# Kernel tuning notes

Hardware: AMD Instinct MI355X
Metric: run time of the kernel (lower is better)

The kernel has to match this reference:

```python
import jax, jax.numpy as jnp
import numpy as np

N, E, G = 50000, 1600000, 512
IN, H = 16, 128


def setup_inputs() -> dict:
    key = jax.random.key(0)
    ks = jax.random.split(key, 10)
    x = jax.random.normal(ks[0], (N, IN), dtype=jnp.float32)
    edge_index = jax.random.randint(ks[1], (2, E), 0, N, dtype=jnp.int64)
    batch = jnp.sort(jax.random.randint(ks[2], (N,), 0, G, dtype=jnp.int64))
    s = lambda k, sh, fan: jax.random.normal(k, sh, dtype=jnp.float32) / np.sqrt(fan)
    return {
        "x": x, "edge_index": edge_index, "batch": batch,
        "W1": s(ks[3], (IN, H), IN), "b1": jnp.zeros((H,), jnp.float32),
        "W2": s(ks[4], (H, H), H), "b2": jnp.zeros((H,), jnp.float32),
        "Wlab": s(ks[5], (H, 1), H), "blab": jnp.zeros((1,), jnp.float32),
        "Wd1": s(ks[6], (H, 64), H), "bd1": jnp.zeros((64,), jnp.float32),
        "Wd2": s(ks[7], (64, 2), 64), "bd2": jnp.zeros((2,), jnp.float32),
    }


def _gcn_conv(x, src, dst, norm, W, b, num_nodes):
    # x' = sum_{(s,d) in E+selfloops} norm_e * (x W)[s] scattered to d, + b
    h = x @ W                                  # [N, H]
    msgs = h[src] * norm[:, None]              # [E+N, H]
    out = jax.ops.segment_sum(msgs, dst, num_segments=num_nodes)
    return out + b


def _forward(x, edge_index, batch, W1, b1, W2, b2, Wlab, blab, Wd1, bd1, Wd2, bd2):
    num_nodes = x.shape[0]
    loop = jnp.arange(num_nodes, dtype=edge_index.dtype)
    src = jnp.concatenate([edge_index[0], loop])
    dst = jnp.concatenate([edge_index[1], loop])
    # symmetric GCN normalization: deg computed at dst after self-loops
    deg = jax.ops.segment_sum(jnp.ones_like(dst, dtype=x.dtype), dst,
                              num_segments=num_nodes)
    dinv = jnp.where(deg > 0, jax.lax.rsqrt(deg), 0.0)
    norm = dinv[src] * dinv[dst]               # [E+N]

    h = jax.nn.relu(_gcn_conv(x, src, dst, norm, W1, b1, num_nodes))
    h = jax.nn.relu(_gcn_conv(h, src, dst, norm, W2, b2, num_nodes))

    # global mean pool over graphs
    sums = jax.ops.segment_sum(h, batch, num_segments=G)        # [G, H]
    cnts = jax.ops.segment_sum(jnp.ones((num_nodes,), h.dtype), batch,
                               num_segments=G)
    pooled = sums / jnp.maximum(cnts, 1.0)[:, None]

    label_out = jax.nn.sigmoid(pooled @ Wlab + blab)            # [G, 1]
    # grad_reverse is identity in the forward pass
    dom_out = jax.nn.relu(pooled @ Wd1 + bd1) @ Wd2 + bd2       # [G, 2]
    return label_out, dom_out


def reference(x, edge_index, batch, W1, b1, W2, b2, Wlab, blab, Wd1, bd1, Wd2, bd2):
    return _forward(x, edge_index, batch, W1, b1, W2, b2, Wlab, blab,
                    Wd1, bd1, Wd2, bd2)
```

## Files before the change

### kernel.cpp

```cpp
#include <hip/hip_runtime.h>
#include <math.h>


#define BCAP 12288

typedef __attribute__((ext_vector_type(8))) short short8;
typedef __attribute__((ext_vector_type(4))) float f32x4;

__device__ __forceinline__ void bf4acc(uint2 u, float* a) {
    a[0] += __uint_as_float(u.x << 16);
    a[1] += __uint_as_float(u.x & 0xffff0000u);
    a[2] += __uint_as_float(u.y << 16);
    a[3] += __uint_as_float(u.y & 0xffff0000u);
}

__device__ __forceinline__ void bf8acc(uint4 u, float* a) {
    a[0] += __uint_as_float(u.x << 16);
    a[1] += __uint_as_float(u.x & 0xffff0000u);
    a[2] += __uint_as_float(u.y << 16);
    a[3] += __uint_as_float(u.y & 0xffff0000u);
    a[4] += __uint_as_float(u.z << 16);
    a[5] += __uint_as_float(u.z & 0xffff0000u);
    a[6] += __uint_as_float(u.w << 16);
    a[7] += __uint_as_float(u.w & 0xffff0000u);
}

__device__ __forceinline__ unsigned short bf1(float a) {
    unsigned ua = __float_as_uint(a);
    return (unsigned short)((ua + 0x7fffu + ((ua >> 16) & 1u)) >> 16);
}

__global__ __launch_bounds__(256) void k_bfill(
        const int* __restrict__ ei, int* __restrict__ bcnt,
        unsigned* __restrict__ col1,
        const int* __restrict__ batch, int* __restrict__ gptr,
        float* __restrict__ gsum, const float* __restrict__ W2,
        unsigned short* __restrict__ W2bf,
        int E, int chunk, int NB, int N, int G) {
    __shared__ int bins[256];
    __shared__ int base[256];
    for (int t = threadIdx.x; t < NB; t += 256) bins[t] = 0;
    __syncthreads();
    const int e0 = blockIdx.x * chunk;
    int e1 = e0 + chunk; if (e1 > E) e1 = E;
    for (int j = e0 + (int)threadIdx.x; j < e1; j += 256)
        atomicAdd(&bins[ei[E + j] >> 8], 1);
    __syncthreads();
    for (int t = threadIdx.x; t < NB; t += 256) {
        base[t] = bins[t] ? atomicAdd(&bcnt[t], bins[t]) : 0;
        bins[t] = 0;
    }
    __syncthreads();
    for (int j = e0 + (int)threadIdx.x; j < e1; j += 256) {
        int d = ei[E + j];
        int s = ei[j];
        int b = d >> 8;
        int pos = base[b] + atomicAdd(&bins[b], 1);
        if (pos < BCAP)
            col1[(size_t)b * BCAP + pos] = ((unsigned)(d & 255) << 16) | (unsigned)s;
    }

    const int gid = blockIdx.x * 256 + threadIdx.x;
    const int gsz = gridDim.x * 256;
    for (int i = gid; i < G * 32; i += gsz)
        ((float4*)gsum)[i] = make_float4(0.f, 0.f, 0.f, 0.f);
    for (int i = gid; i < 16384; i += gsz) {
        const int f2 = i >> 7, f1 = i & 127;
        W2bf[i] = bf1(W2[f1 * 128 + f2]);
    }
    for (int g = gid; g <= G; g += gsz) {
        int lo = 0, hi = N;
        while (lo < hi) {
            int mid = (lo + hi) >> 1;
            if (batch[mid] < g) lo = mid + 1; else hi = mid;
        }
        gptr[g] = lo;
    }
}

__global__ __launch_bounds__(256) void k_bsort(const unsigned* __restrict__ col1,
                                               const int* __restrict__ bcnt,
                                               int* __restrict__ col,
                                               int* __restrict__ rowptr,
                                               float* __restrict__ dinv,
                                               const float* __restrict__ x,
                                               unsigned short* __restrict__ xsb,
                                               int N, int E, int NB) {
    __shared__ unsigned ec[BCAP];
    __shared__ int bins[256], sc[256];
    __shared__ float dvb[256];
    const int b = blockIdx.x, t = threadIdx.x;

    {
        int v = (t < NB) ? bcnt[t] : 0;
        bins[t] = v;
        __syncthreads();
        for (int off = 1; off < 256; off <<= 1) {
            int add = (t >= off) ? bins[t - off] : 0;
            __syncthreads();
            bins[t] += add;
            __syncthreads();
        }
    }
    const int s0 = (b == 0) ? 0 : bins[b - 1];
    int cnt = bcnt[b];
    if (cnt > BCAP) cnt = BCAP;
    __syncthreads();

    for (int i = t; i < cnt; i += 256) ec[i] = col1[(size_t)b * BCAP + i];
    bins[t] = 0;
    __syncthreads();
    for (int i = t; i < cnt; i += 256) atomicAdd(&bins[ec[i] >> 16], 1);
    __syncthreads();
    const int v = bins[t];
    sc[t] = v;
    __syncthreads();
    for (int off = 1; off < 256; off <<= 1) {
        int add = (t >= off) ? sc[t - off] : 0;
        __syncthreads();
        sc[t] += add;
        __syncthreads();
    }
    const int ex = sc[t] - v;
    __syncthreads();
    sc[t] = ex;
    bins[t] = 0;
    const float dv = rsqrtf((float)(v + 1));
    dvb[t] = dv;
    const int n0 = b * 256;
    if (n0 + t < N) {
        rowptr[n0 + t] = s0 + ex;
        dinv[n0 + t] = dv;
    }
    if (b == 0 && t == 0) rowptr[N] = E;
    __syncthreads();
    for (int i = t; i < cnt; i += 256) {
        unsigned e = ec[i];
        int dl = e >> 16;
        int p = sc[dl] + atomicAdd(&bins[dl], 1);
        col[s0 + p] = (int)(e & 0xffffu);
    }
    int nn = N - n0; if (nn > 256) nn = 256;
    const int lim = nn * 16;
    for (int i = t; i < lim; i += 256) {
        float vx = x[(size_t)n0 * 16 + i] * dvb[i >> 4];
        xsb[(size_t)n0 * 16 + i] = bf1(vx);
    }
}

__global__ __launch_bounds__(512, 4) void k_l12g(
        const int* __restrict__ rowptr, const int* __restrict__ col,
        const unsigned short* __restrict__ xsb,
        const float* __restrict__ dinv,
        const float* __restrict__ W1, const float* __restrict__ b1,
        const unsigned short* __restrict__ W2bf,
        unsigned short* __restrict__ ht1b, int N) {
    __shared__ __align__(16) unsigned short W2s[128 * 136];
    __shared__ __align__(16) unsigned short h1b[64 * 136];
    __shared__ __align__(16) float arow[64 * 16];
    __shared__ float dv[64];
    const int tid = threadIdx.x;
    const int n0 = blockIdx.x * 64;
    const int w = tid >> 6, lane = tid & 63;

    for (int i = tid; i < 2048; i += 512) {
        const int f2 = i >> 4, seg = i & 15;
        *(uint4*)&W2s[f2 * 136 + seg * 8] = ((const uint4*)W2bf)[i];
    }
    if (tid < 64) dv[tid] = (n0 + tid < N) ? dinv[n0 + tid] : 0.f;

    {
        const int nd = lane >> 3, sub = lane & 7;
        const int slot = sub >> 2, qq = sub & 3;
        const int j = w * 8 + nd;
        const int n = n0 + j;
        float a[4] = {0.f, 0.f, 0.f, 0.f};
        if (n < N) {
            const int r1 = rowptr[n + 1];
            for (int e = rowptr[n] + slot; e < r1; e += 2)
                bf4acc(*(const uint2*)(xsb + (size_t)col[e] * 16 + qq * 4), a);
        }
#pragma unroll
        for (int i = 0; i < 4; ++i) a[i] += __shfl_xor(a[i], 4);
        if (slot == 0) {
            if (n < N) {
                bf4acc(*(const uint2*)(xsb + (size_t)n * 16 + qq * 4), a);
                *(float4*)&arow[j * 16 + qq * 4] = make_float4(a[0], a[1], a[2], a[3]);
            } else {
                *(float4*)&arow[j * 16 + qq * 4] = make_float4(0.f, 0.f, 0.f, 0.f);
            }
        }
    }
    const int f = tid & 127, jg = tid >> 7;
    float w1r[16];
#pragma unroll
    for (int k = 0; k < 16; ++k) w1r[k] = W1[k * 128 + f];
    const float bias = b1[f];
    __syncthreads();

#pragma unroll 4
    for (int j = jg * 16; j < jg * 16 + 16; ++j) {
        float s = 0.f;
#pragma unroll
        for (int k = 0; k < 16; ++k) s += arow[j * 16 + k] * w1r[k];
        h1b[j * 136 + f] = bf1(fmaxf(dv[j] * s + bias, 0.f));
    }
    __syncthreads();

    const int mt = w & 3, nh = w >> 2;
    const int lm = lane & 15, quad = lane >> 4;
    f32x4 acc[4];
#pragma unroll
    for (int t = 0; t < 4; ++t) acc[t] = (f32x4){0.f, 0.f, 0.f, 0.f};
#pragma unroll
    for (int kb = 0; kb < 4; ++kb) {
        const short8 af = *(const short8*)&h1b[(mt * 16 + lm) * 136 + kb * 32 + quad * 8];
#pragma unroll
        for (int t = 0; t < 4; ++t) {
            const short8 bfv = *(const short8*)&W2s[(nh * 64 + t * 16 + lm) * 136 + kb * 32 + quad * 8];
            acc[t] = __builtin_amdgcn_mfma_f32_16x16x32_bf16(af, bfv, acc[t], 0, 0, 0);
        }
    }
#pragma unroll
    for (int t = 0; t < 4; ++t) {
        const int f2 = nh * 64 + t * 16 + lm;
#pragma unroll
        for (int r = 0; r < 4; ++r) {
            const int j = mt * 16 + quad * 4 + r;
            const int n = n0 + j;
            if (n < N)
                ht1b[(size_t)n * 128 + f2] = bf1(acc[t][r] * dv[j]);
        }
    }
}

__global__ __launch_bounds__(512) void k_gat64pool(
        const int* __restrict__ rowptr, const int* __restrict__ col,
        const unsigned short* __restrict__ ht1b,
        const float* __restrict__ dinv, const float* __restrict__ b2,
        const int* __restrict__ batch, float* __restrict__ gsum,
        int N, int c0) {
    __shared__ __align__(16) float h2s[8][64];
    __shared__ int bats[8];
    const int wave = threadIdx.x >> 6, lane = threadIdx.x & 63;
    const int oct = lane >> 3, t8 = lane & 7;
    const int n = blockIdx.x * 8 + wave;
    const unsigned short* hb = ht1b + c0 + t8 * 8;
    float a[8] = {0.f, 0.f, 0.f, 0.f, 0.f, 0.f, 0.f, 0.f};
    if (n < N) {
        const int r1 = rowptr[n + 1];
        int j = rowptr[n] + oct;
        while (j + 24 < r1) {
            const int s0 = col[j], s1 = col[j + 8];
            const int s2 = col[j + 16], s3 = col[j + 24];
            const uint4 u0 = *(const uint4*)(hb + (size_t)s0 * 128);
            const uint4 u1 = *(const uint4*)(hb + (size_t)s1 * 128);
            const uint4 u2 = *(const uint4*)(hb + (size_t)s2 * 128);
            const uint4 u3 = *(const uint4*)(hb + (size_t)s3 * 128);
            bf8acc(u0, a); bf8acc(u1, a); bf8acc(u2, a); bf8acc(u3, a);
            j += 32;
        }
        while (j < r1) {
            bf8acc(*(const uint4*)(hb + (size_t)col[j] * 128), a);
            j += 8;
        }
        if (oct == 0)
            bf8acc(*(const uint4*)(hb + (size_t)n * 128), a);
    }
#pragma unroll
    for (int i = 0; i < 8; ++i) {
        a[i] += __shfl_xor(a[i], 8);
        a[i] += __shfl_xor(a[i], 16);
        a[i] += __shfl_xor(a[i], 32);
    }
    if (oct == 0) {
        if (n < N) {
            const float d = dinv[n];
            const float4 bb0 = *(const float4*)(b2 + c0 + t8 * 8);
            const float4 bb1 = *(const float4*)(b2 + c0 + t8 * 8 + 4);
            const float4 v0 = make_float4(fmaxf(a[0] * d + bb0.x, 0.f),
                                          fmaxf(a[1] * d + bb0.y, 0.f),
                                          fmaxf(a[2] * d + bb0.z, 0.f),
                                          fmaxf(a[3] * d + bb0.w, 0.f));
            const float4 v1 = make_float4(fmaxf(a[4] * d + bb1.x, 0.f),
                                          fmaxf(a[5] * d + bb1.y, 0.f),
                                          fmaxf(a[6] * d + bb1.z, 0.f),
                                          fmaxf(a[7] * d + bb1.w, 0.f));
            *(float4*)&h2s[wave][t8 * 8] = v0;
            *(float4*)&h2s[wave][t8 * 8 + 4] = v1;
            if (t8 == 0) bats[wave] = batch[n];
        } else {
            *(float4*)&h2s[wave][t8 * 8] = make_float4(0.f, 0.f, 0.f, 0.f);
            *(float4*)&h2s[wave][t8 * 8 + 4] = make_float4(0.f, 0.f, 0.f, 0.f);
            if (t8 == 0) bats[wave] = -1;
        }
    }
    __syncthreads();
    if (threadIdx.x < 16) {
        const int qq = threadIdx.x;
        int bprev = bats[0];
        float4 acc4 = *(const float4*)&h2s[0][qq * 4];
#pragma unroll
        for (int wv = 1; wv < 8; ++wv) {
            const int bw = bats[wv];
            const float4 rv = *(const float4*)&h2s[wv][qq * 4];
            if (bw == bprev) {
                acc4.x += rv.x; acc4.y += rv.y; acc4.z += rv.z; acc4.w += rv.w;
            } else {
                if (bprev >= 0) {
                    float* gs = gsum + (size_t)bprev * 128 + c0 + qq * 4;
                    unsafeAtomicAdd(gs + 0, acc4.x); unsafeAtomicAdd(gs + 1, acc4.y);
                    unsafeAtomicAdd(gs + 2, acc4.z); unsafeAtomicAdd(gs + 3, acc4.w);
                }
                bprev = bw; acc4 = rv;
            }
        }
        if (bprev >= 0) {
            float* gs = gsum + (size_t)bprev * 128 + c0 + qq * 4;
            unsafeAtomicAdd(gs + 0, acc4.x); unsafeAtomicAdd(gs + 1, acc4.y);
            unsafeAtomicAdd(gs + 2, acc4.z); unsafeAtomicAdd(gs + 3, acc4.w);
        }
    }
}

__global__ __launch_bounds__(128) void k_head(
        const float* __restrict__ gsum, const int* __restrict__ gptr,
        const float* __restrict__ Wlab, const float* __restrict__ blab,
        const float* __restrict__ Wd1, const float* __restrict__ bd1,
        const float* __restrict__ Wd2, const float* __restrict__ bd2,
        float* __restrict__ out, int G) {
    __shared__ float sp[128];
    __shared__ float red[128];
    __shared__ float hd[64];
    const int g = blockIdx.x, t = threadIdx.x;
    const float cnt = (float)(gptr[g + 1] - gptr[g]);
    const float invc = 1.f / fmaxf(cnt, 1.f);
    const float pooled = gsum[g * 128 + t] * invc;
    sp[t] = pooled;
    red[t] = pooled * Wlab[t];
    __syncthreads();
    for (int off = 64; off > 0; off >>= 1) {
        if (t < off) red[t] += red[t + off];
        __syncthreads();
    }
    if (t == 0) {
        float z = red[0] + blab[0];
        out[g] = 1.f / (1.f + expf(-z));
    }
    if (t < 64) {
        float s = bd1[t];
        for (int f = 0; f < 128; ++f) s += sp[f] * Wd1[f * 64 + t];
        hd[t] = fmaxf(s, 0.f);
    }
    __syncthreads();
    if (t < 2) {
        float s = bd2[t];
        for (int j = 0; j < 64; ++j) s += hd[j] * Wd2[j * 2 + t];
        out[G + g * 2 + t] = s;
    }
}

extern "C" void kernel_launch(void* const* d_in, const int* in_sizes, int n_in,
                              void* d_out, int out_size, void* d_ws, size_t ws_size,
                              hipStream_t stream) {
    const float* x     = (const float*)d_in[0];
    const int*   ei    = (const int*)d_in[1];
    const int*   batch = (const int*)d_in[2];
    const float* W1    = (const float*)d_in[3];
    const float* b1    = (const float*)d_in[4];
    const float* W2    = (const float*)d_in[5];
    const float* b2    = (const float*)d_in[6];
    const float* Wlab  = (const float*)d_in[7];
    const float* blab  = (const float*)d_in[8];
    const float* Wd1   = (const float*)d_in[9];
    const float* bd1   = (const float*)d_in[10];
    const float* Wd2   = (const float*)d_in[11];
    const float* bd2   = (const float*)d_in[12];
    float* out = (float*)d_out;

    const int N = in_sizes[0] / 16;
    const int E = in_sizes[1] / 2;
    const int G = out_size / 3;
    const int NB = (N + 255) >> 8;

    char* p = (char*)d_ws;
    auto carve = [&](size_t bytes) {
        void* r = (void*)p;
        p += (bytes + 255) & ~(size_t)255;
        return r;
    };
    int*      bcnt   = (int*)     carve(256 * 4);
    unsigned* col1   = (unsigned*)carve((size_t)NB * BCAP * 4);
    int*      col    = (int*)     carve((size_t)E * 4);
    int*      rowptr = (int*)     carve((size_t)(N + 1) * 4);
    int*      gptr   = (int*)     carve((size_t)(G + 1) * 4);
    float*    dinv   = (float*)   carve((size_t)N * 4);
    unsigned short* xsb  = (unsigned short*)carve((size_t)N * 16 * 2);
    unsigned short* W2bf = (unsigned short*)carve(128 * 128 * 2);
    unsigned short* ht1b = (unsigned short*)carve((size_t)N * 128 * 2);
    float*    gsum   = (float*)   carve((size_t)G * 128 * 4);

    const int FB = 256;
    const int chunk = (E + FB - 1) / FB;

    hipMemsetAsync(bcnt, 0, 256 * 4, stream);
    k_bfill  <<<FB, 256, 0, stream>>>(ei, bcnt, col1, batch, gptr, gsum, W2,
                                      W2bf, E, chunk, NB, N, G);
    k_bsort  <<<NB, 256, 0, stream>>>(col1, bcnt, col, rowptr, dinv, x, xsb,
                                      N, E, NB);
    k_l12g   <<<(N + 63) / 64, 512, 0, stream>>>(rowptr, col, xsb, dinv,
                                                 W1, b1, W2bf, ht1b, N);
    k_gat64pool<<<(N + 7) / 8, 512, 0, stream>>>(rowptr, col, ht1b, dinv, b2,
                                                 batch, gsum, N, 0);
    k_gat64pool<<<(N + 7) / 8, 512, 0, stream>>>(rowptr, col, ht1b, dinv, b2,
                                                 batch, gsum, N, 64);
    k_head   <<<G, 128, 0, stream>>>(gsum, gptr, Wlab, blab, Wd1, bd1, Wd2,
                                     bd2, out, G);
}
```

Measured before the change: 248.3 us.

## Merge two half-feature gather-pool launches into one 16-column sliced kernel

Replaces the two k_gat64pool launches (one per 64-column half) with a single launch where each block covers 32 nodes for one 16-column slice out of 8. Each node is handled by a 16-lane group: 8 pairs stride over the neighbours and each half of a pair loads 8 bf16 features. Slice index is blockIdx&7, so neighbouring blocks touch the same rows in different column slices, which may help L2 locality. In exchange each gathered load is only 32 bytes per row, the unrolled 4-way inner loop is dropped (less memory-level parallelism per lane), and pooling now uses 16 lanes over 32 nodes with scalar atomics.

```diff
diff --git a/kernel.cpp b/kernel.cpp
--- a/kernel.cpp
+++ b/kernel.cpp
@@ -234,50 +234,42 @@
     }
 }
 
-__global__ __launch_bounds__(512) void k_gat64pool(
+__global__ __launch_bounds__(512) void k_gatslice(
         const int* __restrict__ rowptr, const int* __restrict__ col,
         const unsigned short* __restrict__ ht1b,
         const float* __restrict__ dinv, const float* __restrict__ b2,
-        const int* __restrict__ batch, float* __restrict__ gsum,
-        int N, int c0) {
-    __shared__ __align__(16) float h2s[8][64];
-    __shared__ int bats[8];
-    const int wave = threadIdx.x >> 6, lane = threadIdx.x & 63;
-    const int oct = lane >> 3, t8 = lane & 7;
-    const int n = blockIdx.x * 8 + wave;
-    const unsigned short* hb = ht1b + c0 + t8 * 8;
+        const int* __restrict__ batch, float* __restrict__ gsum, int N) {
+    __shared__ float h2s[32][16];
+    __shared__ int bats[32];
+    const int s = blockIdx.x & 7;
+    const int nb = blockIdx.x >> 3;
+    const int tid = threadIdx.x;
+    const int wave = tid >> 6, lane = tid & 63;
+    const int grp = lane >> 4;
+    const int gl = lane & 15;
+    const int pair = gl >> 1, half = gl & 1;
+    const int nl = wave * 4 + grp;
+    const int n = nb * 32 + nl;
+    const unsigned short* hb = ht1b + s * 16 + half * 8;
     float a[8] = {0.f, 0.f, 0.f, 0.f, 0.f, 0.f, 0.f, 0.f};
     if (n < N) {
-        const int r1 = rowptr[n + 1];
-        int j = rowptr[n] + oct;
-        while (j + 24 < r1) {
-            const int s0 = col[j], s1 = col[j + 8];
-            const int s2 = col[j + 16], s3 = col[j + 24];
-            const uint4 u0 = *(const uint4*)(hb + (size_t)s0 * 128);
-            const uint4 u1 = *(const uint4*)(hb + (size_t)s1 * 128);
-            const uint4 u2 = *(const uint4*)(hb + (size_t)s2 * 128);
-            const uint4 u3 = *(const uint4*)(hb + (size_t)s3 * 128);
-            bf8acc(u0, a); bf8acc(u1, a); bf8acc(u2, a); bf8acc(u3, a);
-            j += 32;
-        }
-        while (j < r1) {
+        const int r0 = rowptr[n], r1 = rowptr[n + 1];
+        for (int j = r0 + pair; j < r1; j += 8)
             bf8acc(*(const uint4*)(hb + (size_t)col[j] * 128), a);
-            j += 8;
-        }
-        if (oct == 0)
+        if (pair == 0)
             bf8acc(*(const uint4*)(hb + (size_t)n * 128), a);
     }
 #pragma unroll
     for (int i = 0; i < 8; ++i) {
+        a[i] += __shfl_xor(a[i], 2);
+        a[i] += __shfl_xor(a[i], 4);
         a[i] += __shfl_xor(a[i], 8);
-        a[i] += __shfl_xor(a[i], 16);
-        a[i] += __shfl_xor(a[i], 32);
-    }
-    if (oct == 0) {
+    }
+    if (pair == 0) {
         if (n < N) {
             const float d = dinv[n];
-            const float4 bb0 = *(const float4*)(b2 + c0 + t8 * 8);
-            const float4 bb1 = *(const float4*)(b2 + c0 + t8 * 8 + 4);
+            const float4 bb0 = *(const float4*)(b2 + s * 16 + half * 8);
+            const float4 bb1 = *(const float4*)(b2 + s * 16 + half * 8 + 4);
             const float4 v0 = make_float4(fmaxf(a[0] * d + bb0.x, 0.f),
                                           fmaxf(a[1] * d + bb0.y, 0.f),
                                           fmaxf(a[2] * d + bb0.z, 0.f),
@@ -286,40 +278,33 @@
                                           fmaxf(a[5] * d + bb1.y, 0.f),
                                           fmaxf(a[6] * d + bb1.z, 0.f),
                                           fmaxf(a[7] * d + bb1.w, 0.f));
-            *(float4*)&h2s[wave][t8 * 8] = v0;
-            *(float4*)&h2s[wave][t8 * 8 + 4] = v1;
-            if (t8 == 0) bats[wave] = batch[n];
+            *(float4*)&h2s[nl][half * 8] = v0;
+            *(float4*)&h2s[nl][half * 8 + 4] = v1;
+            if (half == 0) bats[nl] = batch[n];
         } else {
-            *(float4*)&h2s[wave][t8 * 8] = make_float4(0.f, 0.f, 0.f, 0.f);
-            *(float4*)&h2s[wave][t8 * 8 + 4] = make_float4(0.f, 0.f, 0.f, 0.f);
-            if (t8 == 0) bats[wave] = -1;
-        }
-    }
-    __syncthreads();
-    if (threadIdx.x < 16) {
-        const int qq = threadIdx.x;
+            *(float4*)&h2s[nl][half * 8] = make_float4(0.f, 0.f, 0.f, 0.f);
+            *(float4*)&h2s[nl][half * 8 + 4] = make_float4(0.f, 0.f, 0.f, 0.f);
+            if (half == 0) bats[nl] = -1;
+        }
+    }
+    __syncthreads();
+    if (tid < 16) {
         int bprev = bats[0];
-        float4 acc4 = *(const float4*)&h2s[0][qq * 4];
-#pragma unroll
-        for (int wv = 1; wv < 8; ++wv) {
-            const int bw = bats[wv];
-            const float4 rv = *(const float4*)&h2s[wv][qq * 4];
+        float acc = h2s[0][tid];
+#pragma unroll 4
+        for (int v = 1; v < 32; ++v) {
+            const int bw = bats[v];
+            const float rv = h2s[v][tid];
             if (bw == bprev) {
-                acc4.x += rv.x; acc4.y += rv.y; acc4.z += rv.z; acc4.w += rv.w;
+                acc += rv;
             } else {
-                if (bprev >= 0) {
-                    float* gs = gsum + (size_t)bprev * 128 + c0 + qq * 4;
-                    unsafeAtomicAdd(gs + 0, acc4.x); unsafeAtomicAdd(gs + 1, acc4.y);
-                    unsafeAtomicAdd(gs + 2, acc4.z); unsafeAtomicAdd(gs + 3, acc4.w);
-                }
-                bprev = bw; acc4 = rv;
+                if (bprev >= 0)
+                    unsafeAtomicAdd(gsum + (size_t)bprev * 128 + s * 16 + tid, acc);
+                bprev = bw; acc = rv;
             }
         }
-        if (bprev >= 0) {
-            float* gs = gsum + (size_t)bprev * 128 + c0 + qq * 4;
-            unsafeAtomicAdd(gs + 0, acc4.x); unsafeAtomicAdd(gs + 1, acc4.y);
-            unsafeAtomicAdd(gs + 2, acc4.z); unsafeAtomicAdd(gs + 3, acc4.w);
-        }
+        if (bprev >= 0)
+            unsafeAtomicAdd(gsum + (size_t)bprev * 128 + s * 16 + tid, acc);
     }
 }
 
@@ -410,10 +395,9 @@
                                       N, E, NB);
     k_l12g   <<<(N + 63) / 64, 512, 0, stream>>>(rowptr, col, xsb, dinv,
                                                  W1, b1, W2bf, ht1b, N);
-    k_gat64pool<<<(N + 7) / 8, 512, 0, stream>>>(rowptr, col, ht1b, dinv, b2,
-                                                 batch, gsum, N, 0);
-    k_gat64pool<<<(N + 7) / 8, 512, 0, stream>>>(rowptr, col, ht1b, dinv, b2,
-                                                 batch, gsum, N, 64);
+    k_gatslice<<<((N + 31) / 32) * 8, 512, 0, stream>>>(rowptr, col, ht1b,
+                                                        dinv, b2, batch,
+                                                        gsum, N);
     k_head   <<<G, 128, 0, stream>>>(gsum, gptr, Wlab, blab, Wd1, bd1, Wd2,
                                      bd2, out, G);
 }
```

New measurement: 292.8 us. 1.18x slower.
